# Kernel tuning notes

Hardware: AMD Instinct MI355X
Metric: run time of the kernel (lower is better)

The kernel has to match this reference:

```python
import math
import jax, jax.numpy as jnp
import numpy as np

B, L, D = 2, 2048, 768
H, DK = 12, 64
NUM_BUCKETS, MAX_DIST = 32, 128


def _relative_position_bucket(rel, bidirectional=True, num_buckets=32, max_distance=128):
    # rel: [Lq, Lk] int32, rel = k_pos - q_pos
    ret = jnp.zeros_like(rel)
    n = -rel
    if bidirectional:
        num_buckets //= 2
        ret = ret + (n < 0).astype(jnp.int32) * num_buckets
        n = jnp.abs(n)
    else:
        n = jnp.maximum(n, 0)
    max_exact = num_buckets // 2
    is_small = n < max_exact
    # safe log: avoid log(0); masked by where(is_small, ...)
    n_safe = jnp.maximum(n, 1).astype(jnp.float32)
    val_if_large = max_exact + (
        jnp.log(n_safe / max_exact) / math.log(max_distance / max_exact) * (num_buckets - max_exact)
    ).astype(jnp.int32)
    val_if_large = jnp.minimum(val_if_large, num_buckets - 1)
    return ret + jnp.where(is_small, n, val_if_large)


def setup_inputs() -> dict:
    key = jax.random.key(0)
    ks = jax.random.split(key, 7)
    s = 1.0 / math.sqrt(D)
    return {
        "query": jax.random.normal(ks[0], (B, L, D), jnp.float32),
        "key_value": jax.random.normal(ks[1], (B, L, D), jnp.float32),
        "key_padding_mask": jnp.ones((B, L), jnp.int32),
        "Wq": jax.random.normal(ks[2], (D, H * DK), jnp.float32) * s,
        "Wk": jax.random.normal(ks[3], (D, H * DK), jnp.float32) * s,
        "Wv": jax.random.normal(ks[4], (D, H * DK), jnp.float32) * s,
        "Wo": jax.random.normal(ks[5], (H * DK, D), jnp.float32) * s,
        "rel_emb": jax.random.normal(ks[6], (NUM_BUCKETS, H), jnp.float32),
    }


def reference(query, key_value, key_padding_mask, Wq, Wk, Wv, Wo, rel_emb):
    Bq, Lq, _ = query.shape
    Lk = key_value.shape[1]
    scale = DK ** (-0.5)

    Q = (query @ Wq).reshape(Bq, Lq, H, DK).transpose(0, 2, 1, 3)      # [B,H,Lq,DK]
    K = (key_value @ Wk).reshape(Bq, Lk, H, DK).transpose(0, 2, 1, 3)  # [B,H,Lk,DK]
    V = (key_value @ Wv).reshape(Bq, Lk, H, DK).transpose(0, 2, 1, 3)

    scores = jnp.einsum("bhqd,bhkd->bhqk", Q, K) * scale               # [B,H,Lq,Lk]

    # T5 relative position bias (bidirectional, causal_mask=False)
    rel = jnp.arange(Lk, dtype=jnp.int32)[None, :] - jnp.arange(Lq, dtype=jnp.int32)[:, None]
    buckets = _relative_position_bucket(rel, True, NUM_BUCKETS, MAX_DIST)  # [Lq,Lk]
    bias = rel_emb[buckets]                                             # [Lq,Lk,H]
    scores = scores + bias.transpose(2, 0, 1)[None]                     # [1,H,Lq,Lk]

    pad = (key_padding_mask == 0)[:, None, None, :]                     # [B,1,1,Lk]
    scores = jnp.where(pad, -jnp.inf, scores)

    attn = jax.nn.softmax(scores.astype(jnp.float32), axis=-1).astype(Q.dtype)
    out = jnp.einsum("bhqk,bhkd->bhqd", attn, V)                        # [B,H,Lq,DK]
    out = out.transpose(0, 2, 1, 3).reshape(Bq, Lq, H * DK)
    return out @ Wo
```

## Files before the change

kernel.cpp:

```cpp
#include <hip/hip_runtime.h>
#include <stdint.h>

typedef __attribute__((ext_vector_type(8))) short bf16x8;
typedef __attribute__((ext_vector_type(4))) float f32x4;
typedef __attribute__((ext_vector_type(4))) unsigned int u32x4;

#define NB 2
#define NL 2048
#define ND 768
#define NH 12
#define NDK 64
#define NM 4096
#define LOG2E 1.4426950408889634f

template<int N> struct IC { static constexpr int v = N; };

__device__ __forceinline__ unsigned short f2bf(float f) {
  unsigned u = __builtin_bit_cast(unsigned, f);
  u += 0x7FFFu + ((u >> 16) & 1u);
  return (unsigned short)(u >> 16);
}

__device__ __forceinline__ float fexp2(float x) {
  float r;
  asm("v_exp_f32 %0, %1" : "=v"(r) : "v"(x));
  return r;
}

__device__ __forceinline__ float xmax32(float x) { return fmaxf(x, __shfl_xor(x, 32)); }
__device__ __forceinline__ float xsum32(float x) { return x + __shfl_xor(x, 32); }

__device__ __forceinline__ void gl_lds16(const unsigned short* g, unsigned short* l) {
  __builtin_amdgcn_global_load_lds((const __attribute__((address_space(1))) void*)g,
                                   (__attribute__((address_space(3))) void*)l, 16, 0, 0);
}

__global__ __launch_bounds__(256) void k_prep(const float* __restrict__ query,
                                              const float* __restrict__ keyval,
                                              const float* __restrict__ Wq,
                                              const float* __restrict__ Wk,
                                              const float* __restrict__ Wv,
                                              const float* __restrict__ Wo,
                                              const float* __restrict__ rel_emb,
                                              const int* __restrict__ mask,
                                              unsigned short* __restrict__ q_bf,
                                              unsigned short* __restrict__ kv_bf,
                                              unsigned short* __restrict__ Wq_t,
                                              unsigned short* __restrict__ Wk_t,
                                              unsigned short* __restrict__ Wv_t,
                                              unsigned short* __restrict__ Wo_t,
                                              float* __restrict__ bias_tab,
                                              float* __restrict__ maskadd,
                                              int* __restrict__ maskall) {
  __shared__ float shbuf[32 * 33];
  int blk = blockIdx.x, tid = threadIdx.x;
  if (blk < 6144) {
    int y = blk / 3072;
    int i = (blk - y * 3072) * 256 + tid;
    const float* src = y ? keyval : query;
    unsigned short* dst = y ? kv_bf : q_bf;
    float4 v = ((const float4*)src)[i];
    ushort4 o;
    o.x = f2bf(v.x); o.y = f2bf(v.y); o.z = f2bf(v.z); o.w = f2bf(v.w);
    ((ushort4*)dst)[i] = o;
  } else if (blk < 8448) {
    int rel = blk - 6144;
    int z = rel / 576, r2 = rel - z * 576;
    int bx = (r2 % 24) * 32, by = (r2 / 24) * 32;
    const float* w = (z == 0) ? Wq : (z == 1) ? Wk : (z == 2) ? Wv : Wo;
    unsigned short* o = (z == 0) ? Wq_t : (z == 1) ? Wk_t : (z == 2) ? Wv_t : Wo_t;
    float scale = (z == 0) ? 0.125f * LOG2E : 1.0f;
    int tx = tid & 31, ty = tid >> 5;
    float (*t)[33] = (float(*)[33])shbuf;
    for (int r = 0; r < 32; r += 8)
      t[ty + r][tx] = w[(by + ty + r) * ND + bx + tx];
    __syncthreads();
    for (int r = 0; r < 32; r += 8)
      o[(bx + ty + r) * ND + by + tx] = f2bf(t[tx][ty + r] * scale);
  } else if (blk < 8640) {
    int idx = (blk - 8448) * 256 + tid;
    if (idx >= 4095 * NH) return;
    int h = idx % NH;
    int di = idx / NH;
    int rel = di - 2047;
    int n = -rel;
    int ret = 0;
    if (n < 0) { ret = 16; n = -n; }
    int b;
    if (n < 8) {
      b = ret + n;
    } else {
      int v = (n >= 91) ? 7 : (n >= 64) ? 6 : (n >= 46) ? 5 : (n >= 32) ? 4
            : (n >= 23) ? 3 : (n >= 16) ? 2 : (n >= 12) ? 1 : 0;
      b = ret + 8 + v;
    }
    bias_tab[h * 4095 + di] = rel_emb[b * NH + h] * LOG2E;
  } else {
    int b = blk - 8640;
    int* red = (int*)shbuf;
    int acc = 1;
    for (int i = tid; i < NL; i += 256) {
      int m = mask[b * NL + i];
      maskadd[b * NL + i] = m ? 0.0f : -1e30f;
      acc &= (m != 0) ? 1 : 0;
    }
    red[tid] = acc;
    __syncthreads();
    for (int s2 = 128; s2 > 0; s2 >>= 1) {
      if (tid < s2) red[tid] &= red[tid + s2];
      __syncthreads();
    }
    if (tid == 0) maskall[b] = red[0];
  }
}

__global__ __launch_bounds__(256) void k_gemm_qkv(const unsigned short* __restrict__ q_bf,
                                                  const unsigned short* __restrict__ kv_bf,
                                                  const unsigned short* __restrict__ Wt,
                                                  unsigned short* __restrict__ Qb,
                                                  unsigned short* __restrict__ Kb,
                                                  unsigned short* __restrict__ Vt) {
  __shared__ unsigned short S[14336];
  unsigned short* As = S;
  unsigned short* Bs = S + 8192;
  int flat = blockIdx.x;
  int nf = (flat & 7) * 96 + (flat >> 3);
  int px = nf / 24;
  int y  = nf - px * 24;
  int tid = threadIdx.x;
  int wave = tid >> 6, lane = tid & 63;
  int lr = lane & 15, lg = lane >> 4;
  int m0 = px * 128;
  int z = y >> 3;
  int nc0 = (y & 7) * 96;
  const unsigned short* A  = (z == 0) ? q_bf : kv_bf;
  const unsigned short* Bt = Wt + (size_t)y * 96 * ND;
  int wm = (wave >> 1) * 64, wn = (wave & 1) * 48;
  int srow = tid >> 3, spc = tid & 7;
  int sg = spc ^ (srow & 7);
  const unsigned short* Ag = A  + (size_t)(m0 + srow) * ND + sg * 8;
  const unsigned short* Bg = Bt + (size_t)srow * ND + sg * 8;
  f32x4 acc[4][3] = {};
  for (int t = 0; t < ND / 64; ++t) {
    int k0 = t * 64;
#pragma unroll
    for (int s = 0; s < 4; ++s)
      gl_lds16(Ag + (size_t)(s * 32) * ND + k0, &As[s * 2048 + tid * 8]);
#pragma unroll
    for (int s = 0; s < 3; ++s)
      gl_lds16(Bg + (size_t)(s * 32) * ND + k0, &Bs[s * 2048 + tid * 8]);
    __syncthreads();
#pragma unroll
    for (int ks = 0; ks < 2; ++ks) {
      bf16x8 af[4], bfr[3];
#pragma unroll
      for (int i = 0; i < 4; ++i) {
        int ar = wm + i * 16 + lr;
        af[i] = *(const bf16x8*)&As[ar * 64 + (((ks * 4 + lg) ^ (ar & 7)) * 8)];
      }
#pragma unroll
      for (int i = 0; i < 3; ++i) {
        int br = wn + i * 16 + lr;
        bfr[i] = *(const bf16x8*)&Bs[br * 64 + (((ks * 4 + lg) ^ (br & 7)) * 8)];
      }
#pragma unroll
      for (int mi = 0; mi < 4; ++mi)
#pragma unroll
        for (int ni = 0; ni < 3; ++ni)
          acc[mi][ni] = __builtin_amdgcn_mfma_f32_16x16x32_bf16(af[mi], bfr[ni], acc[mi][ni], 0, 0, 0);
    }
    __syncthreads();
  }
  if (z == 2) {
    unsigned short* T = S;
#pragma unroll
    for (int mi = 0; mi < 4; ++mi)
#pragma unroll
      for (int ni = 0; ni < 3; ++ni) {
        int col  = wn + ni * 16 + lr;
        int rowb = wm + mi * 16 + lg * 4;
        ushort4 v4;
        v4.x = f2bf(acc[mi][ni][0]);
        v4.y = f2bf(acc[mi][ni][1]);
        v4.z = f2bf(acc[mi][ni][2]);
        v4.w = f2bf(acc[mi][ni][3]);
        int addr = col * 128 + (((rowb >> 3) ^ (col & 7)) * 8) + (rowb & 7);
        *(ushort4*)&T[addr] = v4;
      }
    __syncthreads();
    int bb = m0 >> 11;
    unsigned short* vdst = Vt + (((size_t)bb * ND + nc0) << 11) + (m0 & 2047);
#pragma unroll
    for (int pass = 0; pass < 6; ++pass) {
      int col = (tid >> 4) + pass * 16;
      int cc = tid & 15;
      u32x4 val = *(const u32x4*)&T[col * 128 + ((cc ^ (col & 7)) * 8)];
      *(u32x4*)&vdst[((size_t)col << 11) + cc * 8] = val;
    }
  } else {
#pragma unroll
    for (int mi = 0; mi < 4; ++mi)
#pragma unroll
      for (int ni = 0; ni < 3; ++ni)
#pragma unroll
        for (int r = 0; r < 4; ++r) {
          int row = m0 + wm + mi * 16 + lg * 4 + r;
          int col = nc0 + wn + ni * 16 + lr;
          unsigned short v = f2bf(acc[mi][ni][r]);
          if (z == 0) Qb[(size_t)row * ND + col] = v;
          else        Kb[(size_t)row * ND + col] = v;
        }
  }
}

__global__ __launch_bounds__(256) void k_gemm(const unsigned short* __restrict__ A,
                                              const unsigned short* __restrict__ Bt,
                                              float* __restrict__ Cout,
                                              int Msz, int Nsz, int Ksz) {
  __shared__ unsigned short As[2][4096];
  __shared__ unsigned short Bs[2][4096];
  int flat = blockIdx.x;
  int nf = (flat & 7) * 96 + (flat >> 3);
  int px = nf / 12;
  int y  = nf - px * 12;
  int tid = threadIdx.x;
  int wave = tid >> 6, lane = tid & 63;
  int lr = lane & 15, lg = lane >> 4;
  int m0 = px * 64, n0 = y * 64;
  int wm = (wave >> 1) * 32, wn = (wave & 1) * 32;
  int srow = tid >> 3, spc = tid & 7;
  int sg = spc ^ (srow & 7);
  const unsigned short* Ag = A  + (size_t)(m0 + srow) * Ksz + sg * 8;
  const unsigned short* Bg = Bt + (size_t)(n0 + srow) * Ksz + sg * 8;
  f32x4 acc[2][2] = {};
  const int KT = Ksz >> 6;
#pragma unroll
  for (int s = 0; s < 2; ++s) {
    gl_lds16(Ag + (size_t)(s * 32) * Ksz, &As[0][s * 2048 + tid * 8]);
    gl_lds16(Bg + (size_t)(s * 32) * Ksz, &Bs[0][s * 2048 + tid * 8]);
  }
  __syncthreads();
  int cur = 0;
  for (int t = 0; t < KT; ++t) {
    if (t + 1 < KT) {
      int k0 = (t + 1) << 6;
#pragma unroll
      for (int s = 0; s < 2; ++s) {
        gl_lds16(Ag + (size_t)(s * 32) * Ksz + k0, &As[cur ^ 1][s * 2048 + tid * 8]);
        gl_lds16(Bg + (size_t)(s * 32) * Ksz + k0, &Bs[cur ^ 1][s * 2048 + tid * 8]);
      }
    }
#pragma unroll
    for (int ks = 0; ks < 2; ++ks) {
      bf16x8 af[2], bfr[2];
#pragma unroll
      for (int i = 0; i < 2; ++i) {
        int ar = wm + i * 16 + lr;
        af[i] = *(const bf16x8*)&As[cur][ar * 64 + (((ks * 4 + lg) ^ (ar & 7)) * 8)];
        int br = wn + i * 16 + lr;
        bfr[i] = *(const bf16x8*)&Bs[cur][br * 64 + (((ks * 4 + lg) ^ (br & 7)) * 8)];
      }
#pragma unroll
      for (int mi = 0; mi < 2; ++mi)
#pragma unroll
        for (int ni = 0; ni < 2; ++ni)
          acc[mi][ni] = __builtin_amdgcn_mfma_f32_16x16x32_bf16(af[mi], bfr[ni], acc[mi][ni], 0, 0, 0);
    }
    __syncthreads();
    cur ^= 1;
  }
#pragma unroll
  for (int mi = 0; mi < 2; ++mi)
#pragma unroll
    for (int ni = 0; ni < 2; ++ni)
#pragma unroll
      for (int r = 0; r < 4; ++r) {
        int row = m0 + wm + mi * 16 + lg * 4 + r;
        int col = n0 + wn + ni * 16 + lr;
        Cout[(size_t)row * Nsz + col] = acc[mi][ni][r];
      }
}

__global__ __launch_bounds__(256, 3) void k_attn(const unsigned short* __restrict__ Qb,
                                                 const unsigned short* __restrict__ Kb,
                                                 const unsigned short* __restrict__ Vt,
                                                 const float* __restrict__ bias_tab,
                                                 const float* __restrict__ maskadd,
                                                 const int* __restrict__ maskall,
                                                 unsigned short* __restrict__ Ob) {
  __shared__ unsigned short Ks[3][4096];
  __shared__ unsigned short Vs[3][4096];
  __shared__ float biasw[384];
  int flat = blockIdx.x;
  int nf = (flat & 7) * 96 + (flat >> 3);
  int qt = nf & 31, bh = nf >> 5;
  int b = bh / NH, h = bh % NH;
  int tid = threadIdx.x, wave = tid >> 6, lane = tid & 63;
  int lr = lane & 15, lg = lane >> 4;
  int q0 = qt * 64;
  for (int i = tid; i < 383; i += 256) biasw[i] = bias_tab[h * 4095 + 1856 + i];
  float cFlo = bias_tab[h * 4095];
  float cFhi = bias_tab[h * 4095 + 4094];
  const unsigned short* Kbase = Kb + (size_t)(b * NL) * ND + h * NDK;
  const unsigned short* Vbase = Vt + (size_t)(b * NH + h) * NDK * NL;
  int srow = tid >> 3, spc = tid & 7;
  int sg = spc ^ (srow & 7);
  int l0 = (srow >> 4) * 32 + ((srow >> 2) & 3) * 8 + (srow & 3);
  const unsigned short* Kg0 = Kbase + (size_t)l0 * ND + sg * 8;
  const unsigned short* Kg1 = Kbase + (size_t)(l0 + 4) * ND + sg * 8;
  const unsigned short* Vg0 = Vbase + (size_t)srow * NL + sg * 8;
  const unsigned short* Vg1 = Vbase + (size_t)(32 + srow) * NL + sg * 8;
  bf16x8 aq[2];
  int qw = q0 + wave * 16;
#pragma unroll
  for (int ks = 0; ks < 2; ++ks)
    aq[ks] = *(const bf16x8*)&Qb[(size_t)(b * NL + qw + lr) * ND + h * NDK + ks * 32 + lg * 8];
  const float* cbase = maskadd + b * NL;
  int nomask = __builtin_amdgcn_readfirstlane(maskall[b]);
  f32x4 accO[4] = {};
  float mst = -1e30f, lstl = 0.f;
  int bconst = lg * 8 - wave * 16 - lr + 191 - q0;
  int src0 = (lane & 48) | ((lane >> 2) & 12);
  gl_lds16(Kg0, &Ks[0][tid * 8]);
  gl_lds16(Kg1, &Ks[0][2048 + tid * 8]);
  gl_lds16(Vg0, &Vs[0][tid * 8]);
  gl_lds16(Vg1, &Vs[0][2048 + tid * 8]);
  {
    size_t kok = (size_t)64 * ND, kov = 64;
    gl_lds16(Kg0 + kok, &Ks[1][tid * 8]);
    gl_lds16(Kg1 + kok, &Ks[1][2048 + tid * 8]);
    gl_lds16(Vg0 + kov, &Vs[1][tid * 8]);
    gl_lds16(Vg1 + kov, &Vs[1][2048 + tid * 8]);
  }
  asm volatile("s_waitcnt vmcnt(4) lgkmcnt(0)" ::: "memory");
  __builtin_amdgcn_s_barrier();
  const unsigned short* sk0 = Kg0 + (size_t)2 * 64 * ND;
  const unsigned short* sk1 = Kg1 + (size_t)2 * 64 * ND;
  const unsigned short* sv0 = Vg0 + 2 * 64;
  const unsigned short* sv1 = Vg1 + 2 * 64;

  auto body = [&](int kt_, auto CURc, auto PFc) {
    constexpr int CUR = decltype(CURc)::v;
    constexpr int PF  = decltype(PFc)::v;
    constexpr int ST  = (CUR + 2) % 3;
    float4 cv[2][2];
    if (!nomask) {
#pragma unroll
      for (int hf = 0; hf < 2; ++hf)
#pragma unroll
        for (int qd = 0; qd < 2; ++qd)
          cv[hf][qd] = *(const float4*)&cbase[kt_ * 64 + hf * 32 + lg * 8 + qd * 4];
    }
    if (PF) {
      gl_lds16(sk0, &Ks[ST][tid * 8]);
      gl_lds16(sk1, &Ks[ST][2048 + tid * 8]);
      gl_lds16(sv0, &Vs[ST][tid * 8]);
      gl_lds16(sv1, &Vs[ST][2048 + tid * 8]);
      sk0 += 64 * ND; sk1 += 64 * ND; sv0 += 64; sv1 += 64;
    }
    int kt64 = kt_ * 64;
    bool farlo = (kt64 + 63 < q0 - 90), farhi = (kt64 > q0 + 153);
    float ctile = farlo ? cFlo : (farhi ? cFhi : 0.0f);
    f32x4 s[4];
    __builtin_amdgcn_s_setprio(1);
    if (nomask && (farlo || farhi)) {
      const f32x4 z = {0.f, 0.f, 0.f, 0.f};
#pragma unroll
      for (int ni = 0; ni < 4; ++ni) {
        int kr = ni * 16 + lr;
        bf16x8 bk0 = *(const bf16x8*)&Ks[CUR][kr * 64 + ((lg ^ (lr & 7)) * 8)];
        bf16x8 bk1 = *(const bf16x8*)&Ks[CUR][kr * 64 + (((4 + lg) ^ (lr & 7)) * 8)];
        s[ni] = __builtin_amdgcn_mfma_f32_16x16x32_bf16(bk0, aq[0], z, 0, 0, 0);
        s[ni] = __builtin_amdgcn_mfma_f32_16x16x32_bf16(bk1, aq[1], s[ni], 0, 0, 0);
      }
    } else {
      if (farlo || farhi) {
#pragma unroll
        for (int ni = 0; ni < 4; ++ni)
#pragma unroll
          for (int r = 0; r < 4; ++r) s[ni][r] = 0.f;
      } else {
#pragma unroll
        for (int ni = 0; ni < 4; ++ni)
#pragma unroll
          for (int r = 0; r < 4; ++r)
            s[ni][r] = biasw[kt64 + (ni & 1) * 32 + (ni >> 1) * 4 + r + bconst];
      }
      if (!nomask) {
#pragma unroll
        for (int ni = 0; ni < 4; ++ni)
#pragma unroll
          for (int r = 0; r < 4; ++r)
            s[ni][r] += ((const float*)&cv[ni & 1][ni >> 1])[r];
      }
#pragma unroll
      for (int ni = 0; ni < 4; ++ni) {
        int kr = ni * 16 + lr;
        bf16x8 bk0 = *(const bf16x8*)&Ks[CUR][kr * 64 + ((lg ^ (lr & 7)) * 8)];
        bf16x8 bk1 = *(const bf16x8*)&Ks[CUR][kr * 64 + (((4 + lg) ^ (lr & 7)) * 8)];
        s[ni] = __builtin_amdgcn_mfma_f32_16x16x32_bf16(bk0, aq[0], s[ni], 0, 0, 0);
        s[ni] = __builtin_amdgcn_mfma_f32_16x16x32_bf16(bk1, aq[1], s[ni], 0, 0, 0);
      }
    }
    __builtin_amdgcn_s_setprio(0);
    f32x4 t0, t1;
#pragma unroll
    for (int r = 0; r < 4; ++r) t0[r] = fmaxf(s[0][r], s[1][r]);
#pragma unroll
    for (int r = 0; r < 4; ++r) t1[r] = fmaxf(s[2][r], s[3][r]);
#pragma unroll
    for (int r = 0; r < 4; ++r) t0[r] = fmaxf(t0[r], t1[r]);
    float lm = fmaxf(fmaxf(t0[0], t0[1]), fmaxf(t0[2], t0[3]));
    if (!__all(lm + ctile - mst <= 8.0f)) {
      float pmax = fmaxf(lm, __shfl_xor(lm, 16));
      pmax = xmax32(pmax);
      float pm2 = pmax + ctile;
      float mnew = fmaxf(mst, pm2);
      float sc = fexp2(mst - mnew);
      float scB[4];
#pragma unroll
      for (int r = 0; r < 4; ++r) scB[r] = __shfl(sc, src0 | r);
#pragma unroll
      for (int ni = 0; ni < 4; ++ni)
#pragma unroll
        for (int r = 0; r < 4; ++r) accO[ni][r] *= scB[r];
      lstl *= sc;
      mst = mnew;
    }
    float msub = mst - ctile;
#pragma unroll
    for (int ni = 0; ni < 4; ++ni)
#pragma unroll
      for (int r = 0; r < 4; ++r) s[ni][r] = fexp2(s[ni][r] - msub);
    {
      f32x4 ta = s[0] + s[1];
      f32x4 tb = s[2] + s[3];
      ta = ta + tb;
      lstl += (ta[0] + ta[1]) + (ta[2] + ta[3]);
    }
    unsigned pw[8];
#pragma unroll
    for (int ni = 0; ni < 4; ++ni) {
      unsigned a, c;
      asm("v_cvt_pk_bf16_f32 %0, %1, %2" : "=v"(a) : "v"(s[ni][0]), "v"(s[ni][1]));
      asm("v_cvt_pk_bf16_f32 %0, %1, %2" : "=v"(c) : "v"(s[ni][2]), "v"(s[ni][3]));
      pw[ni * 2] = a; pw[ni * 2 + 1] = c;
    }
    u32x4 apw0 = {pw[0], pw[1], pw[4], pw[5]};
    u32x4 apw1 = {pw[2], pw[3], pw[6], pw[7]};
    bf16x8 ap0 = __builtin_bit_cast(bf16x8, apw0);
    bf16x8 ap1 = __builtin_bit_cast(bf16x8, apw1);
    __builtin_amdgcn_s_setprio(1);
#pragma unroll
    for (int ni = 0; ni < 4; ++ni) {
      int vr = ni * 16 + lr;
      bf16x8 bv0 = *(const bf16x8*)&Vs[CUR][vr * 64 + ((lg ^ (lr & 7)) * 8)];
      bf16x8 bv1 = *(const bf16x8*)&Vs[CUR][vr * 64 + (((4 + lg) ^ (lr & 7)) * 8)];
      accO[ni] = __builtin_amdgcn_mfma_f32_16x16x32_bf16(ap0, bv0, accO[ni], 0, 0, 0);
      accO[ni] = __builtin_amdgcn_mfma_f32_16x16x32_bf16(ap1, bv1, accO[ni], 0, 0, 0);
    }
    __builtin_amdgcn_s_setprio(0);
    if (PF) asm volatile("s_waitcnt vmcnt(4)" ::: "memory");
    else    asm volatile("s_waitcnt vmcnt(0)" ::: "memory");
    __builtin_amdgcn_s_barrier();
  };

  for (int kt = 0; kt < 30; kt += 3) {
    body(kt,     IC<0>{}, IC<1>{});
    body(kt + 1, IC<1>{}, IC<1>{});
    body(kt + 2, IC<2>{}, IC<1>{});
  }
  body(30, IC<0>{}, IC<0>{});
  body(31, IC<1>{}, IC<0>{});

  float lst = lstl + __shfl_xor(lstl, 16);
  lst = xsum32(lst);
  float linv = 1.0f / lst;
  float lB[4];
#pragma unroll
  for (int r = 0; r < 4; ++r) lB[r] = __shfl(linv, src0 | r);
#pragma unroll
  for (int ni = 0; ni < 4; ++ni)
#pragma unroll
    for (int r = 0; r < 4; ++r) {
      int qg = qw + lg * 4 + r;
      int col = h * NDK + ni * 16 + lr;
      Ob[(size_t)(b * NL + qg) * ND + col] = f2bf(accO[ni][r] * lB[r]);
    }
}

extern "C" void kernel_launch(void* const* d_in, const int* in_sizes, int n_in,
                              void* d_out, int out_size, void* d_ws, size_t ws_size,
                              hipStream_t stream) {
  const float* query  = (const float*)d_in[0];
  const float* keyval = (const float*)d_in[1];
  const int*   mask   = (const int*)d_in[2];
  const float* Wq     = (const float*)d_in[3];
  const float* Wk     = (const float*)d_in[4];
  const float* Wv     = (const float*)d_in[5];
  const float* Wo     = (const float*)d_in[6];
  const float* rel    = (const float*)d_in[7];

  char* ws = (char*)d_ws;
  unsigned short* q_bf  = (unsigned short*)(ws);
  unsigned short* kv_bf = (unsigned short*)(ws + 6291456);
  unsigned short* Wq_t  = (unsigned short*)(ws + 12582912);
  unsigned short* Wk_t  = (unsigned short*)(ws + 13762560);
  unsigned short* Wv_t  = (unsigned short*)(ws + 14942208);
  unsigned short* Wo_t  = (unsigned short*)(ws + 16121856);
  unsigned short* Qb    = (unsigned short*)(ws + 17301504);
  unsigned short* Kb    = (unsigned short*)(ws + 23592960);
  unsigned short* Vt    = (unsigned short*)(ws + 29884416);
  unsigned short* Ob    = (unsigned short*)(ws + 36175872);
  float* bias_tab       = (float*)(ws + 42467328);
  float* maskadd        = (float*)(ws + 42663936);
  int*   maskall        = (int*)(ws + 42680320);

  k_prep<<<dim3(8642), dim3(256), 0, stream>>>(query, keyval, Wq, Wk, Wv, Wo, rel, mask,
                                               q_bf, kv_bf, Wq_t, Wk_t, Wv_t, Wo_t,
                                               bias_tab, maskadd, maskall);
  k_gemm_qkv<<<dim3(768), dim3(256), 0, stream>>>(q_bf, kv_bf, Wq_t, Qb, Kb, Vt);
  k_attn<<<dim3(768), dim3(256), 0, stream>>>(Qb, Kb, Vt, bias_tab, maskadd, maskall, Ob);
  k_gemm<<<dim3(768), dim3(256), 0, stream>>>(Ob, Wo_t, (float*)d_out, NM, ND, ND);
}
```

Measured before the change: 93.18 us.

## Fuse fp32-to-bf16 activation conversion into QKV GEMM A-tile loads

Drops the separate prep pass that converted query and key_value to bf16 in a workspace. The QKV GEMM now reads fp32 activations directly, converts them in registers and writes them into the swizzled LDS tile, while B still uses async global-to-LDS loads. This removes a full write and re-read of the bf16 activation copies, but the A loads become synchronous register round-trips, read twice the bytes per tile, and are repeated by each of the 24 column blocks. The max reduction in the attention kernel is also reassociated into a flatter tree.

```diff
diff --git a/kernel.cpp b/kernel.cpp
--- a/kernel.cpp
+++ b/kernel.cpp
@@ -35,16 +35,12 @@
                                    (__attribute__((address_space(3))) void*)l, 16, 0, 0);
 }
 
-__global__ __launch_bounds__(256) void k_prep(const float* __restrict__ query,
-                                              const float* __restrict__ keyval,
-                                              const float* __restrict__ Wq,
+__global__ __launch_bounds__(256) void k_prep(const float* __restrict__ Wq,
                                               const float* __restrict__ Wk,
                                               const float* __restrict__ Wv,
                                               const float* __restrict__ Wo,
                                               const float* __restrict__ rel_emb,
                                               const int* __restrict__ mask,
-                                              unsigned short* __restrict__ q_bf,
-                                              unsigned short* __restrict__ kv_bf,
                                               unsigned short* __restrict__ Wq_t,
                                               unsigned short* __restrict__ Wk_t,
                                               unsigned short* __restrict__ Wv_t,
@@ -54,18 +50,8 @@
                                               int* __restrict__ maskall) {
   __shared__ float shbuf[32 * 33];
   int blk = blockIdx.x, tid = threadIdx.x;
-  if (blk < 6144) {
-    int y = blk / 3072;
-    int i = (blk - y * 3072) * 256 + tid;
-    const float* src = y ? keyval : query;
-    unsigned short* dst = y ? kv_bf : q_bf;
-    float4 v = ((const float4*)src)[i];
-    ushort4 o;
-    o.x = f2bf(v.x); o.y = f2bf(v.y); o.z = f2bf(v.z); o.w = f2bf(v.w);
-    ((ushort4*)dst)[i] = o;
-  } else if (blk < 8448) {
-    int rel = blk - 6144;
-    int z = rel / 576, r2 = rel - z * 576;
+  if (blk < 2304) {
+    int z = blk / 576, r2 = blk - z * 576;
     int bx = (r2 % 24) * 32, by = (r2 / 24) * 32;
     const float* w = (z == 0) ? Wq : (z == 1) ? Wk : (z == 2) ? Wv : Wo;
     unsigned short* o = (z == 0) ? Wq_t : (z == 1) ? Wk_t : (z == 2) ? Wv_t : Wo_t;
@@ -77,8 +63,8 @@
     __syncthreads();
     for (int r = 0; r < 32; r += 8)
       o[(bx + ty + r) * ND + by + tx] = f2bf(t[tx][ty + r] * scale);
-  } else if (blk < 8640) {
-    int idx = (blk - 8448) * 256 + tid;
+  } else if (blk < 2496) {
+    int idx = (blk - 2304) * 256 + tid;
     if (idx >= 4095 * NH) return;
     int h = idx % NH;
     int di = idx / NH;
@@ -96,7 +82,7 @@
     }
     bias_tab[h * 4095 + di] = rel_emb[b * NH + h] * LOG2E;
   } else {
-    int b = blk - 8640;
+    int b = blk - 2496;
     int* red = (int*)shbuf;
     int acc = 1;
     for (int i = tid; i < NL; i += 256) {
@@ -114,8 +100,8 @@
   }
 }
 
-__global__ __launch_bounds__(256) void k_gemm_qkv(const unsigned short* __restrict__ q_bf,
-                                                  const unsigned short* __restrict__ kv_bf,
+__global__ __launch_bounds__(256) void k_gemm_qkv(const float* __restrict__ qf,
+                                                  const float* __restrict__ kvf,
                                                   const unsigned short* __restrict__ Wt,
                                                   unsigned short* __restrict__ Qb,
                                                   unsigned short* __restrict__ Kb,
@@ -133,22 +119,30 @@
   int m0 = px * 128;
   int z = y >> 3;
   int nc0 = (y & 7) * 96;
-  const unsigned short* A  = (z == 0) ? q_bf : kv_bf;
+  const float* A32 = (z == 0) ? qf : kvf;
   const unsigned short* Bt = Wt + (size_t)y * 96 * ND;
   int wm = (wave >> 1) * 64, wn = (wave & 1) * 48;
   int srow = tid >> 3, spc = tid & 7;
   int sg = spc ^ (srow & 7);
-  const unsigned short* Ag = A  + (size_t)(m0 + srow) * ND + sg * 8;
+  const float* Agf = A32 + (size_t)(m0 + srow) * ND + sg * 8;
   const unsigned short* Bg = Bt + (size_t)srow * ND + sg * 8;
   f32x4 acc[4][3] = {};
   for (int t = 0; t < ND / 64; ++t) {
     int k0 = t * 64;
 #pragma unroll
-    for (int s = 0; s < 4; ++s)
-      gl_lds16(Ag + (size_t)(s * 32) * ND + k0, &As[s * 2048 + tid * 8]);
-#pragma unroll
     for (int s = 0; s < 3; ++s)
       gl_lds16(Bg + (size_t)(s * 32) * ND + k0, &Bs[s * 2048 + tid * 8]);
+#pragma unroll
+    for (int s = 0; s < 4; ++s) {
+      const float4* p = (const float4*)(Agf + (size_t)(s * 32) * ND + k0);
+      float4 a0 = p[0], a1 = p[1];
+      ushort4 u0, u1;
+      u0.x = f2bf(a0.x); u0.y = f2bf(a0.y); u0.z = f2bf(a0.z); u0.w = f2bf(a0.w);
+      u1.x = f2bf(a1.x); u1.y = f2bf(a1.y); u1.z = f2bf(a1.z); u1.w = f2bf(a1.w);
+      int rl = s * 32 + srow;
+      *(ushort4*)&As[rl * 64 + spc * 8]     = u0;
+      *(ushort4*)&As[rl * 64 + spc * 8 + 4] = u1;
+    }
     __syncthreads();
 #pragma unroll
     for (int ks = 0; ks < 2; ++ks) {
@@ -403,14 +397,12 @@
       }
     }
     __builtin_amdgcn_s_setprio(0);
-    f32x4 t0, t1;
-#pragma unroll
-    for (int r = 0; r < 4; ++r) t0[r] = fmaxf(s[0][r], s[1][r]);
-#pragma unroll
-    for (int r = 0; r < 4; ++r) t1[r] = fmaxf(s[2][r], s[3][r]);
-#pragma unroll
-    for (int r = 0; r < 4; ++r) t0[r] = fmaxf(t0[r], t1[r]);
-    float lm = fmaxf(fmaxf(t0[0], t0[1]), fmaxf(t0[2], t0[3]));
+    float a0 = fmaxf(fmaxf(s[0][0], s[0][1]), s[0][2]);
+    float a1 = fmaxf(fmaxf(s[0][3], s[1][0]), s[1][1]);
+    float a2 = fmaxf(fmaxf(s[1][2], s[1][3]), s[2][0]);
+    float a3 = fmaxf(fmaxf(s[2][1], s[2][2]), s[2][3]);
+    float a4 = fmaxf(fmaxf(s[3][0], s[3][1]), s[3][2]);
+    float lm = fmaxf(fmaxf(fmaxf(a0, a1), a2), fmaxf(fmaxf(a3, a4), s[3][3]));
     if (!__all(lm + ctile - mst <= 8.0f)) {
       float pmax = fmaxf(lm, __shfl_xor(lm, 16));
       pmax = xmax32(pmax);
@@ -502,8 +494,6 @@
   const float* rel    = (const float*)d_in[7];
 
   char* ws = (char*)d_ws;
-  unsigned short* q_bf  = (unsigned short*)(ws);
-  unsigned short* kv_bf = (unsigned short*)(ws + 6291456);
   unsigned short* Wq_t  = (unsigned short*)(ws + 12582912);
   unsigned short* Wk_t  = (unsigned short*)(ws + 13762560);
   unsigned short* Wv_t  = (unsigned short*)(ws + 14942208);
@@ -516,10 +506,10 @@
   float* maskadd        = (float*)(ws + 42663936);
   int*   maskall        = (int*)(ws + 42680320);
 
-  k_prep<<<dim3(8642), dim3(256), 0, stream>>>(query, keyval, Wq, Wk, Wv, Wo, rel, mask,
-                                               q_bf, kv_bf, Wq_t, Wk_t, Wv_t, Wo_t,
+  k_prep<<<dim3(2498), dim3(256), 0, stream>>>(Wq, Wk, Wv, Wo, rel, mask,
+                                               Wq_t, Wk_t, Wv_t, Wo_t,
                                                bias_tab, maskadd, maskall);
-  k_gemm_qkv<<<dim3(768), dim3(256), 0, stream>>>(q_bf, kv_bf, Wq_t, Qb, Kb, Vt);
+  k_gemm_qkv<<<dim3(768), dim3(256), 0, stream>>>(query, keyval, Wq_t, Qb, Kb, Vt);
   k_attn<<<dim3(768), dim3(256), 0, stream>>>(Qb, Kb, Vt, bias_tab, maskadd, maskall, Ob);
   k_gemm<<<dim3(768), dim3(256), 0, stream>>>(Ob, Wo_t, (float*)d_out, NM, ND, ND);
 }
```

Measured after the change: 98.72 us. 1.06x slower.
